# Optimization experiments

Measured on AMD Instinct MI355X. Metric: run time of the kernel, lower is better.

The kernel has to match this reference:

```python
import jax, jax.numpy as jnp
import numpy as np
from jax import lax

VOCAB, D, H, K = 20000, 100, 100, 3
N_U, N_I, R, S, E = 256, 256, 8, 52, 20000


def _text_processor(reviews, emb_table, conv_w, conv_b):
    # reviews: [B,R,S] int -> c: [B,R,S',H]
    B, Rr, Ss = reviews.shape
    embs = emb_table[reviews]                              # [B,R,S,D]
    x = embs.reshape(B * Rr, 1, Ss, D)                     # NCHW
    c = lax.conv_general_dilated(x, conv_w, (1, 1), 'VALID',
                                 dimension_numbers=('NCHW', 'OIHW', 'NCHW'))
    c = jax.nn.relu(c + conv_b[None, :, None, None])       # [B*R,H,S',1]
    Sp = Ss - K + 1
    c = c[..., 0].transpose(0, 2, 1).reshape(B, Rr, Sp, H) # [B,R,S',H]
    return c


def _branch(reviews, emb_table, conv_w, conv_b, fc_w_w, fc_w_b, fc_w2_w, fc_w2_b):
    c = _text_processor(reviews, emb_table, conv_w, conv_b)
    rho = jax.nn.sigmoid(c @ fc_w_w.T + fc_w_b)            # [B,R,S',1]
    z = rho + lax.stop_gradient(jnp.round(rho) - rho)      # straight-through round
    z = z[..., 0]                                          # [B,R,S']
    P = jnp.max(c, axis=-2) @ fc_w2_w.T + fc_w2_b          # [B,R,D]
    return P, z


def reference(user_reviews, item_reviews, uid, iid, emb_table, conv_w, conv_b,
              fc_w_w, fc_w_b, fc_w2_w, fc_w2_b, h_r_w, h_c_w,
              user_bias, item_bias, global_bias):
    P_u, z_u = _branch(user_reviews, emb_table, conv_w, conv_b, fc_w_w, fc_w_b, fc_w2_w, fc_w2_b)
    P_i, z_i = _branch(item_reviews, emb_table, conv_w, conv_b, fc_w_w, fc_w_b, fc_w2_w, fc_w2_b)
    Pu, Pi = P_u[uid], P_i[iid]                            # edge gathers [E,R,D]
    zu, zi = z_u[uid], z_i[iid]                            # [E,R,S']
    s_uv = jnp.einsum('eud,evd->euv', Pu, Pi)              # per-edge review similarity [E,R,R]
    rho_u = jax.nn.sigmoid(s_uv.sum(-1))                   # [E,R]
    rho_v = jax.nn.sigmoid(s_uv.sum(-2))                   # [E,R]
    gamma_u_r = jnp.einsum('ers,er->es', zu, rho_u)        # [E,S']
    gamma_v_r = jnp.einsum('ers,er->es', zi, rho_v)
    pred_r = (jnp.concatenate([gamma_u_r, gamma_v_r], -1) @ h_r_w.T
              + user_bias[uid] + item_bias[iid] + global_bias)  # [E,1]
    gamma_u_c = jnp.einsum('er,erd->ed', rho_u, Pu)        # [E,D]
    gamma_v_c = jnp.einsum('er,erd->ed', rho_v, Pi)
    pred_c = jnp.concatenate([gamma_u_c, gamma_v_c], -1) @ h_c_w.T  # [E,1]
    return pred_r, pred_c, z_u, z_i


def setup_inputs() -> dict:
    key = jax.random.key(0)
    ks = jax.random.split(key, 12)
    return {
        'user_reviews': jax.random.randint(ks[0], (N_U, R, S), 0, VOCAB, dtype=jnp.int32),
        'item_reviews': jax.random.randint(ks[1], (N_I, R, S), 0, VOCAB, dtype=jnp.int32),
        'uid': jax.random.randint(ks[2], (E,), 0, N_U, dtype=jnp.int32),
        'iid': jax.random.randint(ks[3], (E,), 0, N_I, dtype=jnp.int32),
        'emb_table': jax.random.normal(ks[4], (VOCAB, D), jnp.float32) * 0.1,
        'conv_w': jax.random.normal(ks[5], (H, 1, K, D), jnp.float32) * 0.05,
        'conv_b': jnp.zeros((H,), jnp.float32),
        'fc_w_w': jax.random.normal(ks[6], (1, H), jnp.float32) * 0.1,
        'fc_w_b': jnp.zeros((1,), jnp.float32),
        'fc_w2_w': jax.random.normal(ks[7], (D, H), jnp.float32) * 0.1,
        'fc_w2_b': jnp.zeros((D,), jnp.float32),
        'h_r_w': jax.random.normal(ks[8], (1, 2 * (S - K + 1)), jnp.float32) * 0.1,
        'h_c_w': jax.random.normal(ks[9], (1, 2 * D), jnp.float32) * 0.1,
        'user_bias': jnp.zeros((N_U, 1), jnp.float32),
        'item_bias': jnp.zeros((N_I, 1), jnp.float32),
        'global_bias': jnp.zeros((1,), jnp.float32),
    }
```

## Files before the change

kernel.cpp:

```cpp
#include <hip/hip_runtime.h>
#include <hip/hip_fp16.h>
#include <math.h>


typedef __attribute__((ext_vector_type(8))) _Float16 half8;
typedef __attribute__((ext_vector_type(4))) float f32x4;

__device__ __forceinline__ float sigmoidf_(float x) { return 1.f / (1.f + expf(-x)); }
__device__ __forceinline__ ushort f2h(float x) {
    union { __half h; ushort u; } t; t.h = __float2half(x); return t.u;
}
__device__ __forceinline__ float h2f(ushort u) {
    union { __half h; ushort u; } t; t.u = u; return __half2float(t.h);
}

#define Z_MARGIN 4e-4f
#define FLAG_CAP 204800

__global__ void k_prep(const float* __restrict__ conv_w, const float* __restrict__ fc_w2_w,
                       const float* __restrict__ emb,
                       float* __restrict__ Wt, float* __restrict__ fc2t,
                       float* __restrict__ Psum, ushort* __restrict__ wpack,
                       int* __restrict__ flag_cnt, ushort* __restrict__ emb16) {
    int idx = blockIdx.x * 256 + threadIdx.x;
    if (idx < 30000) {
        int kk = idx / 100, h = idx - kk * 100;
        Wt[idx] = conv_w[h * 300 + kk];
    } else if (idx < 40000) {
        int j = idx - 30000;
        int h = j / 100, dd = j - h * 100;
        fc2t[j] = fc_w2_w[dd * 100 + h];
    } else if (idx < 91200) {
        Psum[idx - 40000] = 0.f;
    } else if (idx < 127040) {
        int j = idx - 91200;
        int frag = j >> 9, within = j & 511;
        int l = within >> 3, jj = within & 7;
        int kt = frag / 7, nt = frag % 7;
        int kk = kt * 32 + ((l >> 4) << 3) + jj;
        int h  = nt * 16 + (l & 15);
        wpack[j] = (kk < 300 && h < 100) ? f2h(conv_w[h * 300 + kk]) : (ushort)0;
    } else if (idx == 127040) {
        *flag_cnt = 0;
    } else {
        int j = idx - 127041;
        if (j < 500000) {
            float4 v = ((const float4*)emb)[j];
            uint2 o;
            o.x = (unsigned)f2h(v.x) | ((unsigned)f2h(v.y) << 16);
            o.y = (unsigned)f2h(v.z) | ((unsigned)f2h(v.w) << 16);
            ((uint2*)emb16)[j] = o;
        }
    }
}

__global__ __launch_bounds__(256, 6)
void k_branch(const int* __restrict__ u_rev, const int* __restrict__ i_rev,
              const ushort* __restrict__ emb16, const ushort* __restrict__ wpack,
              const float* __restrict__ conv_b, const float* __restrict__ fc_w_w,
              const float* __restrict__ fc_w_b, const float* __restrict__ fc_w2_b,
              const float* __restrict__ fc2t, const float* __restrict__ h_r_w,
              const float* __restrict__ h_c_w,
              float* __restrict__ Pbuf, float* __restrict__ Psum,
              float* __restrict__ zdot, float* __restrict__ Pdot,
              float* __restrict__ z_out, int* __restrict__ flag_cnt,
              int* __restrict__ flag_list) {
    __shared__ __align__(16) char smem[23552];
    ushort* xw    = (ushort*)smem;
    ushort* wbuf  = (ushort*)(smem + 13312);
    int*    s_tok = (int*)(smem + 20480);
    float*  s_vmax= (float*)(smem + 20688);
    float*  s_maxf= (float*)(smem + 22288);
    float*  s_z   = (float*)(smem + 22688);
    float*  s_lg  = (float*)(smem + 22896);
    float*  s_P   = (float*)(smem + 23104);

    const int tid = threadIdx.x, lane = tid & 63, w = tid >> 6;
    const int gi = blockIdx.x;
    const int branch = gi >> 11, inst = gi & 2047;

    const uint4* wp4 = (const uint4*)wpack;
    uint4* wbuf4 = (uint4*)wbuf;
    uint4 st0 = wp4[tid];
    uint4 st1; if (tid < 192) st1 = wp4[256 + tid];

    const int* rev = branch ? i_rev : u_rev;
    if (tid < 52) s_tok[tid] = rev[inst * 52 + tid];
    __syncthreads();

    {
        const uint2* emb2 = (const uint2*)emb16;
        uint2 v[6];
#pragma unroll
        for (int k = 0; k < 6; k++) {
            int idx = tid + (k << 8);
            if (idx < 1300) {
                int s = idx / 25, c = idx - s * 25;
                v[k] = emb2[s_tok[s] * 25 + c];
            }
        }
#pragma unroll
        for (int k = 0; k < 6; k++) {
            int idx = tid + (k << 8);
            if (idx < 1300) *(uint2*)(xw + idx * 4) = v[k];
        }
        uint4 z4; z4.x = 0u; z4.y = 0u; z4.z = 0u; z4.w = 0u;
        for (int t2 = tid; t2 < 182; t2 += 256)
            ((uint4*)xw)[650 + t2] = z4;
    }

    wbuf4[tid] = st0;
    if (tid < 192) wbuf4[256 + tid] = st1;
    st0 = wp4[448 + tid];
    if (tid < 192) st1 = wp4[448 + 256 + tid];
    __syncthreads();

    f32x4 acc[7];
#pragma unroll
    for (int nt = 0; nt < 7; nt++) acc[nt] = (f32x4){0.f, 0.f, 0.f, 0.f};

    const int col = lane & 15, quad = lane >> 4, q8 = quad << 3;
    const int mt = w;

    for (int kt = 0; kt < 10; kt++) {
        {
            int e0 = (mt * 16 + col) * 100 + kt * 32 + q8;
            union AU { half8 h8; uint2 u2[2]; } a;
            a.u2[0] = *(const uint2*)(xw + e0);
            a.u2[1] = *(const uint2*)(xw + e0 + 4);
#pragma unroll
            for (int nt = 0; nt < 7; nt++) {
                union BU { half8 h8; uint4 u4; } b;
                b.u4 = wbuf4[nt * 64 + lane];
                acc[nt] = __builtin_amdgcn_mfma_f32_16x16x32_f16(a.h8, b.h8, acc[nt], 0, 0, 0);
            }
        }
        __syncthreads();
        if (kt < 9) {
            wbuf4[tid] = st0;
            if (tid < 192) wbuf4[256 + tid] = st1;
            if (kt < 8) {
                st0 = wp4[(kt + 2) * 448 + tid];
                if (tid < 192) st1 = wp4[(kt + 2) * 448 + 256 + tid];
            }
            __syncthreads();
        }
    }

    float cb[7], fw[7], vmax[7];
#pragma unroll
    for (int nt = 0; nt < 7; nt++) {
        int h = nt * 16 + col;
        cb[nt] = (h < 100) ? conv_b[h] : 0.f;
        fw[nt] = (h < 100) ? fc_w_w[h] : 0.f;
        vmax[nt] = 0.f;
    }
    const float fcb = fc_w_b[0];

#pragma unroll
    for (int j = 0; j < 4; j++) {
        int p = mt * 16 + quad * 4 + j;
        bool pv = p < 50;
        float part = 0.f;
#pragma unroll
        for (int nt = 0; nt < 7; nt++) {
            float c = acc[nt][j] + cb[nt];
            c = c > 0.f ? c : 0.f;
            part += c * fw[nt];
            if (pv) vmax[nt] = fmaxf(vmax[nt], c);
        }
        part += __shfl_xor(part, 1, 64);
        part += __shfl_xor(part, 2, 64);
        part += __shfl_xor(part, 4, 64);
        part += __shfl_xor(part, 8, 64);
        if (pv && col == 0) {
            float logit = part + fcb;
            float z = rintf(sigmoidf_(logit));
            s_z[p] = z;
            s_lg[p] = logit;
            z_out[branch * 102400 + inst * 50 + p] = z;
        }
    }

#pragma unroll
    for (int nt = 0; nt < 7; nt++) {
        float m = vmax[nt];
        m = fmaxf(m, __shfl_xor(m, 16, 64));
        m = fmaxf(m, __shfl_xor(m, 32, 64));
        int h = nt * 16 + col;
        if (quad == 0 && h < 100) s_vmax[w * 100 + h] = m;
    }
    __syncthreads();

    if (tid < 100) {
        float mx = fmaxf(fmaxf(s_vmax[tid], s_vmax[100 + tid]),
                         fmaxf(s_vmax[200 + tid], s_vmax[300 + tid]));
        s_maxf[tid] = mx;
    }
    __syncthreads();

    if (tid < 100) {
        float a = fc_w2_b[tid];
        for (int h0 = 0; h0 < 100; h0 += 10) {
            float wv[10], mxv[10];
#pragma unroll
            for (int t = 0; t < 10; t++) {
                wv[t] = fc2t[(h0 + t) * 100 + tid];
                mxv[t] = s_maxf[h0 + t];
            }
#pragma unroll
            for (int t = 0; t < 10; t++) a += mxv[t] * wv[t];
        }
        Pbuf[gi * 100 + tid] = a;
        s_P[tid] = a;
        atomicAdd(&Psum[(branch * 256 + (inst >> 3)) * 100 + tid], a);
    }
    __syncthreads();

    if (w == 0) {
        float v = (lane < 50) ? s_z[lane] * h_r_w[branch * 50 + lane] : 0.f;
        for (int s = 1; s < 64; s <<= 1) v += __shfl_xor(v, s, 64);
        if (lane == 0) zdot[gi] = v;
    } else if (w == 1) {
        float u = 0.f;
        if (lane < 50) u = s_P[lane] * h_c_w[branch * 100 + lane]
                         + s_P[lane + 50] * h_c_w[branch * 100 + lane + 50];
        for (int s = 1; s < 64; s <<= 1) u += __shfl_xor(u, s, 64);
        if (lane == 0) Pdot[gi] = u;
    } else if (w == 2) {
        float lg = 1e9f;
        if (lane < 50) lg = s_lg[lane];
        unsigned long long mb = __ballot(fabsf(lg) < Z_MARGIN);
        int cnt = __popcll(mb);
        int base = 0;
        if (lane == 0 && cnt) base = atomicAdd(flag_cnt, cnt);
        base = __shfl(base, 0, 64);
        if (fabsf(lg) < Z_MARGIN) {
            int rank = __popcll(mb & ((1ull << lane) - 1ull));
            int k = base + rank;
            if (k < FLAG_CAP) flag_list[k] = gi * 50 + lane;
        }
    }
}

__launch_bounds__(256)
__global__ void k_refine(const int* __restrict__ u_rev, const int* __restrict__ i_rev,
                         const float* __restrict__ emb, const float* __restrict__ Wt,
                         const float* __restrict__ conv_b, const float* __restrict__ fc_w_w,
                         const float* __restrict__ fc_w_b, const float* __restrict__ h_r_w,
                         const int* __restrict__ flag_cnt, const int* __restrict__ flag_list,
                         float* __restrict__ z_out, float* __restrict__ zdot) {
    int n = *flag_cnt; if (n > FLAG_CAP) n = FLAG_CAP;
    const int lane = threadIdx.x & 63;
    const int wid = (blockIdx.x * 256 + threadIdx.x) >> 6;
    const int nw = gridDim.x * 4;
    const bool hv = lane < 50;
    const float cb0 = hv ? conv_b[lane] : 0.f;
    const float cb1 = hv ? conv_b[lane + 50] : 0.f;
    const float fw0 = hv ? fc_w_w[lane] : 0.f;
    const float fw1 = hv ? fc_w_w[lane + 50] : 0.f;
    const float fcb = fc_w_b[0];

    for (int e0 = wid * 4; e0 < n; e0 += nw * 4) {
        int gi[4], pos[4];
        bool iv[4];
        float xr[4][5];
#pragma unroll
        for (int m = 0; m < 4; m++) {
            int e = e0 + m;
            iv[m] = e < n;
            int code = iv[m] ? flag_list[e] : 0;
            gi[m] = code / 50; pos[m] = code - gi[m] * 50;
            const int* rev = (gi[m] >> 11) ? i_rev : u_rev;
            int tb = (gi[m] & 2047) * 52 + pos[m];
            int t0 = rev[tb], t1 = rev[tb + 1], t2 = rev[tb + 2];
#pragma unroll
            for (int s = 0; s < 5; s++) {
                int k = s * 64 + lane;
                float v = 0.f;
                if (k < 300) {
                    int r = k / 100, dd = k - r * 100;
                    int t = (r == 0) ? t0 : ((r == 1) ? t1 : t2);
                    v = emb[t * 100 + dd];
                }
                xr[m][s] = v;
            }
        }
        float c0[4], c1[4];
#pragma unroll
        for (int m = 0; m < 4; m++) { c0[m] = cb0; c1[m] = cb1; }
        for (int s = 0; s < 5; s++) {
            const int dmax = (s < 4) ? 64 : 44;
            for (int db = 0; db < dmax; db += 16) {
                const int cnt = (dmax - db < 16) ? (dmax - db) : 16;
                float w0a[16], w1a[16];
#pragma unroll
                for (int t = 0; t < 16; t++) {
                    int d = s * 64 + db + t;
                    bool on = (t < cnt) && hv;
                    w0a[t] = on ? Wt[d * 100 + lane] : 0.f;
                    w1a[t] = on ? Wt[d * 100 + lane + 50] : 0.f;
                }
#pragma unroll
                for (int t = 0; t < 16; t++) {
#pragma unroll
                    for (int m = 0; m < 4; m++) {
                        float x = __shfl(xr[m][s], db + t, 64);
                        c0[m] += x * w0a[t];
                        c1[m] += x * w1a[t];
                    }
                }
            }
        }
#pragma unroll
        for (int m = 0; m < 4; m++) {
            float v = fmaxf(c0[m], 0.f) * fw0 + fmaxf(c1[m], 0.f) * fw1;
            for (int s = 1; s < 64; s <<= 1) v += __shfl_xor(v, s, 64);
            if (lane == 0 && iv[m]) {
                int branch = gi[m] >> 11, inst = gi[m] & 2047;
                float z = rintf(sigmoidf_(v + fcb));
                float old = z_out[branch * 102400 + inst * 50 + pos[m]];
                if (z != old) {
                    z_out[branch * 102400 + inst * 50 + pos[m]] = z;
                    atomicAdd(&zdot[gi[m]], (z - old) * h_r_w[branch * 50 + pos[m]]);
                }
            }
        }
    }
}

__launch_bounds__(256)
__global__ void k_gmat(const float* __restrict__ Pbuf, const float* __restrict__ Psum,
                       ushort* __restrict__ G) {
    __shared__ __align__(16) float sv[100];
    const int b = blockIdx.x, s = b >> 11, i = (b >> 3) & 255, jc = b & 7;
    const int tid = threadIdx.x, lane = tid & 63, w = tid >> 6;
    const float* vec = Psum + (s == 0 ? 25600 : 0) + i * 100;
    if (tid < 100) sv[tid] = vec[tid];
    __syncthreads();
    const int g = lane >> 2, q = lane & 3;
    const float4* rows4 = (const float4*)(Pbuf + s * 204800);
    const float4* sv4 = (const float4*)sv;
    for (int pass = 0; pass < 4; pass++) {
        int j = jc * 256 + pass * 64 + w * 16 + g;
        float part = 0.f;
#pragma unroll
        for (int t = 0; t < 7; t++) {
            int c = q + 4 * t;
            if (c < 25) {
                float4 a = rows4[j * 25 + c], bb = sv4[c];
                part += a.x * bb.x + a.y * bb.y + a.z * bb.z + a.w * bb.w;
            }
        }
        part += __shfl_xor(part, 1, 64);
        part += __shfl_xor(part, 2, 64);
        if (q == 0) G[s * 524288 + i * 2048 + j] = f2h(part);
    }
}

__launch_bounds__(256)
__global__ void k_edge(const int* __restrict__ uid, const int* __restrict__ iid,
                       const ushort* __restrict__ G,
                       const float* __restrict__ zdot, const float* __restrict__ Pdot,
                       const float* __restrict__ user_bias, const float* __restrict__ item_bias,
                       const float* __restrict__ global_bias, float* __restrict__ out) {
    const int tid = threadIdx.x, lane = tid & 63, w = tid >> 6;
    const int e = blockIdx.x * 16 + w * 4 + (lane >> 4);
    const int r = lane & 15;
    int u = uid[e], i = iid[e];
    float gv, wr, wc;
    if (r < 8) {
        gv = h2f(G[i * 2048 + u * 8 + r]);
        wr = zdot[u * 8 + r]; wc = Pdot[u * 8 + r];
    } else {
        int a = r - 8;
        gv = h2f(G[524288 + u * 2048 + i * 8 + a]);
        wr = zdot[2048 + i * 8 + a]; wc = Pdot[2048 + i * 8 + a];
    }
    float sg = sigmoidf_(gv);
    float cr = sg * wr, cc = sg * wc;
    cr += __shfl_xor(cr, 1, 64); cc += __shfl_xor(cc, 1, 64);
    cr += __shfl_xor(cr, 2, 64); cc += __shfl_xor(cc, 2, 64);
    cr += __shfl_xor(cr, 4, 64); cc += __shfl_xor(cc, 4, 64);
    cr += __shfl_xor(cr, 8, 64); cc += __shfl_xor(cc, 8, 64);
    if (r == 0) {
        out[e] = cr + user_bias[u] + item_bias[i] + global_bias[0];
        out[20000 + e] = cc;
    }
}

extern "C" void kernel_launch(void* const* d_in, const int* in_sizes, int n_in,
                              void* d_out, int out_size, void* d_ws, size_t ws_size,
                              hipStream_t stream) {
    const int*   u_rev    = (const int*)d_in[0];
    const int*   i_rev    = (const int*)d_in[1];
    const int*   uid      = (const int*)d_in[2];
    const int*   iid      = (const int*)d_in[3];
    const float* emb      = (const float*)d_in[4];
    const float* conv_w   = (const float*)d_in[5];
    const float* conv_b   = (const float*)d_in[6];
    const float* fc_w_w   = (const float*)d_in[7];
    const float* fc_w_b   = (const float*)d_in[8];
    const float* fc_w2_w  = (const float*)d_in[9];
    const float* fc_w2_b  = (const float*)d_in[10];
    const float* h_r_w    = (const float*)d_in[11];
    const float* h_c_w    = (const float*)d_in[12];
    const float* user_b   = (const float*)d_in[13];
    const float* item_b   = (const float*)d_in[14];
    const float* global_b = (const float*)d_in[15];
    float* out = (float*)d_out;

    float*  ws    = (float*)d_ws;
    float*  Pbuf  = ws;
    float*  Psum  = ws + 409600;
    float*  zdotb = ws + 460800;
    float*  Pdotb = ws + 464896;
    float*  Wt    = ws + 468992;
    float*  fc2t  = ws + 498992;
    ushort* wpack = (ushort*)(ws + 508992);
    int*    flagc = (int*)(ws + 526912);
    int*    flist = (int*)(ws + 526916);
    ushort* emb16 = (ushort*)(ws + 731716);
    ushort* Gbuf  = (ushort*)(ws + 1731716);

    hipLaunchKernelGGL(k_prep, dim3(2450), dim3(256), 0, stream,
                       conv_w, fc_w2_w, emb, Wt, fc2t, Psum, wpack, flagc, emb16);
    hipLaunchKernelGGL(k_branch, dim3(4096), dim3(256), 0, stream,
                       u_rev, i_rev, emb16, wpack, conv_b, fc_w_w, fc_w_b,
                       fc_w2_b, fc2t, h_r_w, h_c_w,
                       Pbuf, Psum, zdotb, Pdotb, out + 40000, flagc, flist);
    hipLaunchKernelGGL(k_refine, dim3(128), dim3(256), 0, stream,
                       u_rev, i_rev, emb, Wt, conv_b, fc_w_w, fc_w_b, h_r_w,
                       flagc, flist, out + 40000, zdotb);
    hipLaunchKernelGGL(k_gmat, dim3(4096), dim3(256), 0, stream, Pbuf, Psum, Gbuf);
    hipLaunchKernelGGL(k_edge, dim3(1250), dim3(256), 0, stream,
                       uid, iid, Gbuf, zdotb, Pdotb,
                       user_b, item_b, global_b, out);
}
```

Measured before the change: 189.2 us.

## Load conv weight fragments directly into registers, dropping LDS staging and barriers

The MFMA B-operand weight fragments are now read straight from global memory (L2/L1-resident) into double-buffered register arrays, prefetching the next k-tile while computing the current one. This removes the LDS weight buffer and the two block-wide barriers per k-step, which shrinks shared memory from 23.5KB to 16KB. Launch bounds drop from 6 to 4 waves per SIMD to leave room for the 14 extra uint4 registers, trading occupancy for fewer syncs. Each wave now fetches the full weight set redundantly from cache.

Measured after the change: 205.3 us. 1.09x slower.

```diff
diff --git a/kernel.cpp b/kernel.cpp
--- a/kernel.cpp
+++ b/kernel.cpp
@@ -54,7 +54,7 @@
     }
 }
 
-__global__ __launch_bounds__(256, 6)
+__global__ __launch_bounds__(256, 4)
 void k_branch(const int* __restrict__ u_rev, const int* __restrict__ i_rev,
               const ushort* __restrict__ emb16, const ushort* __restrict__ wpack,
               const float* __restrict__ conv_b, const float* __restrict__ fc_w_w,
@@ -65,24 +65,20 @@
               float* __restrict__ zdot, float* __restrict__ Pdot,
               float* __restrict__ z_out, int* __restrict__ flag_cnt,
               int* __restrict__ flag_list) {
-    __shared__ __align__(16) char smem[23552];
+    __shared__ __align__(16) char smem[16384];
     ushort* xw    = (ushort*)smem;
-    ushort* wbuf  = (ushort*)(smem + 13312);
-    int*    s_tok = (int*)(smem + 20480);
-    float*  s_vmax= (float*)(smem + 20688);
-    float*  s_maxf= (float*)(smem + 22288);
-    float*  s_z   = (float*)(smem + 22688);
-    float*  s_lg  = (float*)(smem + 22896);
-    float*  s_P   = (float*)(smem + 23104);
+    int*    s_tok = (int*)(smem + 13312);
+    float*  s_vmax= (float*)(smem + 13520);
+    float*  s_maxf= (float*)(smem + 15120);
+    float*  s_z   = (float*)(smem + 15520);
+    float*  s_lg  = (float*)(smem + 15728);
+    float*  s_P   = (float*)(smem + 15936);
 
     const int tid = threadIdx.x, lane = tid & 63, w = tid >> 6;
     const int gi = blockIdx.x;
     const int branch = gi >> 11, inst = gi & 2047;
 
     const uint4* wp4 = (const uint4*)wpack;
-    uint4* wbuf4 = (uint4*)wbuf;
-    uint4 st0 = wp4[tid];
-    uint4 st1; if (tid < 192) st1 = wp4[256 + tid];
 
     const int* rev = branch ? i_rev : u_rev;
     if (tid < 52) s_tok[tid] = rev[inst * 52 + tid];
@@ -108,11 +104,6 @@
         for (int t2 = tid; t2 < 182; t2 += 256)
             ((uint4*)xw)[650 + t2] = z4;
     }
-
-    wbuf4[tid] = st0;
-    if (tid < 192) wbuf4[256 + tid] = st1;
-    st0 = wp4[448 + tid];
-    if (tid < 192) st1 = wp4[448 + 256 + tid];
     __syncthreads();
 
     f32x4 acc[7];
@@ -122,30 +113,41 @@
     const int col = lane & 15, quad = lane >> 4, q8 = quad << 3;
     const int mt = w;
 
-    for (int kt = 0; kt < 10; kt++) {
-        {
-            int e0 = (mt * 16 + col) * 100 + kt * 32 + q8;
-            union AU { half8 h8; uint2 u2[2]; } a;
-            a.u2[0] = *(const uint2*)(xw + e0);
-            a.u2[1] = *(const uint2*)(xw + e0 + 4);
-#pragma unroll
-            for (int nt = 0; nt < 7; nt++) {
-                union BU { half8 h8; uint4 u4; } b;
-                b.u4 = wbuf4[nt * 64 + lane];
-                acc[nt] = __builtin_amdgcn_mfma_f32_16x16x32_f16(a.h8, b.h8, acc[nt], 0, 0, 0);
-            }
-        }
-        __syncthreads();
-        if (kt < 9) {
-            wbuf4[tid] = st0;
-            if (tid < 192) wbuf4[256 + tid] = st1;
-            if (kt < 8) {
-                st0 = wp4[(kt + 2) * 448 + tid];
-                if (tid < 192) st1 = wp4[(kt + 2) * 448 + 256 + tid];
-            }
-            __syncthreads();
-        }
-    }
+    uint4 bA[7], bB[7];
+#pragma unroll
+    for (int nt = 0; nt < 7; nt++) bA[nt] = wp4[nt * 64 + lane];
+
+#define KT_BODY(KT, CUR, NXT)                                                   \
+    {                                                                           \
+        if ((KT) < 9) {                                                         \
+            _Pragma("unroll")                                                   \
+            for (int nt = 0; nt < 7; nt++)                                      \
+                NXT[nt] = wp4[((KT) + 1) * 448 + nt * 64 + lane];               \
+        }                                                                       \
+        int e0 = (mt * 16 + col) * 100 + (KT) * 32 + q8;                        \
+        union AU { half8 h8; uint2 u2[2]; } a;                                  \
+        a.u2[0] = *(const uint2*)(xw + e0);                                     \
+        a.u2[1] = *(const uint2*)(xw + e0 + 4);                                 \
+        _Pragma("unroll")                                                       \
+        for (int nt = 0; nt < 7; nt++) {                                        \
+            union BV { half8 h8; uint4 u4; } b;                                 \
+            b.u4 = CUR[nt];                                                     \
+            acc[nt] = __builtin_amdgcn_mfma_f32_16x16x32_f16(a.h8, b.h8,        \
+                                                             acc[nt], 0, 0, 0); \
+        }                                                                       \
+    }
+
+    KT_BODY(0, bA, bB)
+    KT_BODY(1, bB, bA)
+    KT_BODY(2, bA, bB)
+    KT_BODY(3, bB, bA)
+    KT_BODY(4, bA, bB)
+    KT_BODY(5, bB, bA)
+    KT_BODY(6, bA, bB)
+    KT_BODY(7, bB, bA)
+    KT_BODY(8, bA, bB)
+    KT_BODY(9, bB, bA)
+#undef KT_BODY
 
     float cb[7], fw[7], vmax[7];
 #pragma unroll
```

## Process two review instances per k_branch block to reuse staged conv weights

Applied to the files above, without the earlier changes.

Each k_branch block now handles two review instances instead of one, so the grid is halved. The fp16 conv weight tiles staged into LDS are loaded once and feed MFMAs for both instances, which halves global weight traffic and barrier count per instance. In exchange the block needs roughly twice the LDS and twice the accumulator registers, and launch bounds drop to 4 waves-per-EU, so occupancy falls.

Measured after the change: 184.9 us. 1.02x faster.

```diff
diff --git a/kernel.cpp b/kernel.cpp
--- a/kernel.cpp
+++ b/kernel.cpp
@@ -54,7 +54,7 @@
     }
 }
 
-__global__ __launch_bounds__(256, 6)
+__global__ __launch_bounds__(256, 4)
 void k_branch(const int* __restrict__ u_rev, const int* __restrict__ i_rev,
               const ushort* __restrict__ emb16, const ushort* __restrict__ wpack,
               const float* __restrict__ conv_b, const float* __restrict__ fc_w_w,
@@ -65,19 +65,20 @@
               float* __restrict__ zdot, float* __restrict__ Pdot,
               float* __restrict__ z_out, int* __restrict__ flag_cnt,
               int* __restrict__ flag_list) {
-    __shared__ __align__(16) char smem[23552];
+    __shared__ __align__(16) char smem[39840];
     ushort* xw    = (ushort*)smem;
-    ushort* wbuf  = (ushort*)(smem + 13312);
-    int*    s_tok = (int*)(smem + 20480);
-    float*  s_vmax= (float*)(smem + 20688);
-    float*  s_maxf= (float*)(smem + 22288);
-    float*  s_z   = (float*)(smem + 22688);
-    float*  s_lg  = (float*)(smem + 22896);
-    float*  s_P   = (float*)(smem + 23104);
+    ushort* wbuf  = (ushort*)(smem + 26624);
+    int*    s_tok = (int*)(smem + 33792);
+    float*  s_vmax= (float*)(smem + 34208);
+    float*  s_maxf= (float*)(smem + 37408);
+    float*  s_z   = (float*)(smem + 38208);
+    float*  s_lg  = (float*)(smem + 38624);
+    float*  s_P   = (float*)(smem + 39040);
 
     const int tid = threadIdx.x, lane = tid & 63, w = tid >> 6;
-    const int gi = blockIdx.x;
-    const int branch = gi >> 11, inst = gi & 2047;
+    const int b = blockIdx.x;
+    const int branch = b >> 10, pair = b & 1023;
+    const int inst0 = pair * 2;
 
     const uint4* wp4 = (const uint4*)wpack;
     uint4* wbuf4 = (uint4*)wbuf;
@@ -85,28 +86,39 @@
     uint4 st1; if (tid < 192) st1 = wp4[256 + tid];
 
     const int* rev = branch ? i_rev : u_rev;
-    if (tid < 52) s_tok[tid] = rev[inst * 52 + tid];
+    if (tid < 104) {
+        int ii = tid >= 52, s = tid - ii * 52;
+        s_tok[tid] = rev[(inst0 + ii) * 52 + s];
+    }
     __syncthreads();
 
     {
         const uint2* emb2 = (const uint2*)emb16;
-        uint2 v[6];
-#pragma unroll
-        for (int k = 0; k < 6; k++) {
+        uint2 v[11];
+#pragma unroll
+        for (int k = 0; k < 11; k++) {
             int idx = tid + (k << 8);
-            if (idx < 1300) {
-                int s = idx / 25, c = idx - s * 25;
-                v[k] = emb2[s_tok[s] * 25 + c];
-            }
-        }
-#pragma unroll
-        for (int k = 0; k < 6; k++) {
+            if (idx < 2600) {
+                int ii = idx >= 1300;
+                int within = idx - ii * 1300;
+                int s = within / 25, c = within - s * 25;
+                v[k] = emb2[s_tok[ii * 52 + s] * 25 + c];
+            }
+        }
+#pragma unroll
+        for (int k = 0; k < 11; k++) {
             int idx = tid + (k << 8);
-            if (idx < 1300) *(uint2*)(xw + idx * 4) = v[k];
+            if (idx < 2600) {
+                int ii = idx >= 1300;
+                int within = idx - ii * 1300;
+                *(uint2*)(xw + ii * 6656 + within * 4) = v[k];
+            }
         }
         uint4 z4; z4.x = 0u; z4.y = 0u; z4.z = 0u; z4.w = 0u;
-        for (int t2 = tid; t2 < 182; t2 += 256)
-            ((uint4*)xw)[650 + t2] = z4;
+        for (int t2 = tid; t2 < 364; t2 += 256) {
+            int ii = t2 >= 182, off = t2 - ii * 182;
+            ((uint4*)xw)[ii * 832 + 650 + off] = z4;
+        }
     }
 
     wbuf4[tid] = st0;
@@ -115,9 +127,12 @@
     if (tid < 192) st1 = wp4[448 + 256 + tid];
     __syncthreads();
 
-    f32x4 acc[7];
-#pragma unroll
-    for (int nt = 0; nt < 7; nt++) acc[nt] = (f32x4){0.f, 0.f, 0.f, 0.f};
+    f32x4 acc0[7], acc1[7];
+#pragma unroll
+    for (int nt = 0; nt < 7; nt++) {
+        acc0[nt] = (f32x4){0.f, 0.f, 0.f, 0.f};
+        acc1[nt] = (f32x4){0.f, 0.f, 0.f, 0.f};
+    }
 
     const int col = lane & 15, quad = lane >> 4, q8 = quad << 3;
     const int mt = w;
@@ -125,14 +140,17 @@
     for (int kt = 0; kt < 10; kt++) {
         {
             int e0 = (mt * 16 + col) * 100 + kt * 32 + q8;
-            union AU { half8 h8; uint2 u2[2]; } a;
-            a.u2[0] = *(const uint2*)(xw + e0);
-            a.u2[1] = *(const uint2*)(xw + e0 + 4);
+            union AU { half8 h8; uint2 u2[2]; } a0, a1;
+            a0.u2[0] = *(const uint2*)(xw + e0);
+            a0.u2[1] = *(const uint2*)(xw + e0 + 4);
+            a1.u2[0] = *(const uint2*)(xw + 6656 + e0);
+            a1.u2[1] = *(const uint2*)(xw + 6656 + e0 + 4);
 #pragma unroll
             for (int nt = 0; nt < 7; nt++) {
-                union BU { half8 h8; uint4 u4; } b;
-                b.u4 = wbuf4[nt * 64 + lane];
-                acc[nt] = __builtin_amdgcn_mfma_f32_16x16x32_f16(a.h8, b.h8, acc[nt], 0, 0, 0);
+                union BU { half8 h8; uint4 u4; } bu;
+                bu.u4 = wbuf4[nt * 64 + lane];
+                acc0[nt] = __builtin_amdgcn_mfma_f32_16x16x32_f16(a0.h8, bu.h8, acc0[nt], 0, 0, 0);
+                acc1[nt] = __builtin_amdgcn_mfma_f32_16x16x32_f16(a1.h8, bu.h8, acc1[nt], 0, 0, 0);
             }
         }
         __syncthreads();
@@ -147,89 +165,108 @@
         }
     }
 
-    float cb[7], fw[7], vmax[7];
+    float cb[7], fw[7];
 #pragma unroll
     for (int nt = 0; nt < 7; nt++) {
         int h = nt * 16 + col;
         cb[nt] = (h < 100) ? conv_b[h] : 0.f;
         fw[nt] = (h < 100) ? fc_w_w[h] : 0.f;
-        vmax[nt] = 0.f;
     }
     const float fcb = fc_w_b[0];
 
-#pragma unroll
-    for (int j = 0; j < 4; j++) {
-        int p = mt * 16 + quad * 4 + j;
-        bool pv = p < 50;
-        float part = 0.f;
-#pragma unroll
-        for (int nt = 0; nt < 7; nt++) {
-            float c = acc[nt][j] + cb[nt];
-            c = c > 0.f ? c : 0.f;
-            part += c * fw[nt];
-            if (pv) vmax[nt] = fmaxf(vmax[nt], c);
-        }
-        part += __shfl_xor(part, 1, 64);
-        part += __shfl_xor(part, 2, 64);
-        part += __shfl_xor(part, 4, 64);
-        part += __shfl_xor(part, 8, 64);
-        if (pv && col == 0) {
-            float logit = part + fcb;
-            float z = rintf(sigmoidf_(logit));
-            s_z[p] = z;
-            s_lg[p] = logit;
-            z_out[branch * 102400 + inst * 50 + p] = z;
-        }
-    }
-
-#pragma unroll
-    for (int nt = 0; nt < 7; nt++) {
-        float m = vmax[nt];
-        m = fmaxf(m, __shfl_xor(m, 16, 64));
-        m = fmaxf(m, __shfl_xor(m, 32, 64));
-        int h = nt * 16 + col;
-        if (quad == 0 && h < 100) s_vmax[w * 100 + h] = m;
-    }
-    __syncthreads();
-
-    if (tid < 100) {
-        float mx = fmaxf(fmaxf(s_vmax[tid], s_vmax[100 + tid]),
-                         fmaxf(s_vmax[200 + tid], s_vmax[300 + tid]));
-        s_maxf[tid] = mx;
-    }
-    __syncthreads();
-
-    if (tid < 100) {
-        float a = fc_w2_b[tid];
+#define EPILOGUE_MM(II, ACC)                                                   \
+    {                                                                          \
+        float vmax[7];                                                         \
+        _Pragma("unroll") for (int nt = 0; nt < 7; nt++) vmax[nt] = 0.f;       \
+        _Pragma("unroll")                                                      \
+        for (int j = 0; j < 4; j++) {                                          \
+            int p = mt * 16 + quad * 4 + j;                                    \
+            bool pv = p < 50;                                                  \
+            float part = 0.f;                                                  \
+            _Pragma("unroll")                                                  \
+            for (int nt = 0; nt < 7; nt++) {                                   \
+                float c = ACC[nt][j] + cb[nt];                                 \
+                c = c > 0.f ? c : 0.f;                                         \
+                part += c * fw[nt];                                            \
+                if (pv) vmax[nt] = fmaxf(vmax[nt], c);                         \
+            }                                                                  \
+            part += __shfl_xor(part, 1, 64);                                   \
+            part += __shfl_xor(part, 2, 64);                                   \
+            part += __shfl_xor(part, 4, 64);                                   \
+            part += __shfl_xor(part, 8, 64);                                   \
+            if (pv && col == 0) {                                              \
+                float logit = part + fcb;                                      \
+                float z = rintf(sigmoidf_(logit));                             \
+                s_z[(II) * 52 + p] = z;                                        \
+                s_lg[(II) * 52 + p] = logit;                                   \
+                z_out[branch * 102400 + (inst0 + (II)) * 50 + p] = z;          \
+            }                                                                  \
+        }                                                                      \
+        _Pragma("unroll")                                                      \
+        for (int nt = 0; nt < 7; nt++) {                                       \
+            float m = vmax[nt];                                                \
+            m = fmaxf(m, __shfl_xor(m, 16, 64));                               \
+            m = fmaxf(m, __shfl_xor(m, 32, 64));                               \
+            int h = nt * 16 + col;                                             \
+            if (quad == 0 && h < 100) s_vmax[(II) * 400 + w * 100 + h] = m;    \
+        }                                                                      \
+    }
+
+    EPILOGUE_MM(0, acc0)
+    EPILOGUE_MM(1, acc1)
+#undef EPILOGUE_MM
+    __syncthreads();
+
+    if (tid < 200) {
+        int ii = tid >= 100, h = tid - ii * 100;
+        const float* sv = s_vmax + ii * 400;
+        float mx = fmaxf(fmaxf(sv[h], sv[100 + h]),
+                         fmaxf(sv[200 + h], sv[300 + h]));
+        s_maxf[ii * 100 + h] = mx;
+    }
+    __syncthreads();
+
+    if (tid < 200) {
+        int ii = tid >= 100, dd = tid - ii * 100;
+        float a = fc_w2_b[dd];
         for (int h0 = 0; h0 < 100; h0 += 10) {
             float wv[10], mxv[10];
 #pragma unroll
             for (int t = 0; t < 10; t++) {
-                wv[t] = fc2t[(h0 + t) * 100 + tid];
-                mxv[t] = s_maxf[h0 + t];
+                wv[t] = fc2t[(h0 + t) * 100 + dd];
+                mxv[t] = s_maxf[ii * 100 + h0 + t];
             }
 #pragma unroll
             for (int t = 0; t < 10; t++) a += mxv[t] * wv[t];
         }
-        Pbuf[gi * 100 + tid] = a;
-        s_P[tid] = a;
-        atomicAdd(&Psum[(branch * 256 + (inst >> 3)) * 100 + tid], a);
+        int inst = inst0 + ii;
+        int gi = branch * 2048 + inst;
+        Pbuf[gi * 100 + dd] = a;
+        s_P[ii * 100 + dd] = a;
+        atomicAdd(&Psum[(branch * 256 + (inst >> 3)) * 100 + dd], a);
     }
     __syncthreads();
 
     if (w == 0) {
-        float v = (lane < 50) ? s_z[lane] * h_r_w[branch * 50 + lane] : 0.f;
-        for (int s = 1; s < 64; s <<= 1) v += __shfl_xor(v, s, 64);
-        if (lane == 0) zdot[gi] = v;
+#pragma unroll
+        for (int ii = 0; ii < 2; ii++) {
+            float v = (lane < 50) ? s_z[ii * 52 + lane] * h_r_w[branch * 50 + lane] : 0.f;
+            for (int s = 1; s < 64; s <<= 1) v += __shfl_xor(v, s, 64);
+            if (lane == 0) zdot[branch * 2048 + inst0 + ii] = v;
+        }
     } else if (w == 1) {
-        float u = 0.f;
-        if (lane < 50) u = s_P[lane] * h_c_w[branch * 100 + lane]
-                         + s_P[lane + 50] * h_c_w[branch * 100 + lane + 50];
-        for (int s = 1; s < 64; s <<= 1) u += __shfl_xor(u, s, 64);
-        if (lane == 0) Pdot[gi] = u;
-    } else if (w == 2) {
+#pragma unroll
+        for (int ii = 0; ii < 2; ii++) {
+            float u = 0.f;
+            if (lane < 50) u = s_P[ii * 100 + lane] * h_c_w[branch * 100 + lane]
+                             + s_P[ii * 100 + lane + 50] * h_c_w[branch * 100 + lane + 50];
+            for (int s = 1; s < 64; s <<= 1) u += __shfl_xor(u, s, 64);
+            if (lane == 0) Pdot[branch * 2048 + inst0 + ii] = u;
+        }
+    } else {
+        int ii = w - 2;
         float lg = 1e9f;
-        if (lane < 50) lg = s_lg[lane];
+        if (lane < 50) lg = s_lg[ii * 52 + lane];
         unsigned long long mb = __ballot(fabsf(lg) < Z_MARGIN);
         int cnt = __popcll(mb);
         int base = 0;
@@ -238,7 +275,7 @@
         if (fabsf(lg) < Z_MARGIN) {
             int rank = __popcll(mb & ((1ull << lane) - 1ull));
             int k = base + rank;
-            if (k < FLAG_CAP) flag_list[k] = gi * 50 + lane;
+            if (k < FLAG_CAP) flag_list[k] = (branch * 2048 + inst0 + ii) * 50 + lane;
         }
     }
 }
@@ -425,7 +462,7 @@
 
     hipLaunchKernelGGL(k_prep, dim3(2450), dim3(256), 0, stream,
                        conv_w, fc_w2_w, emb, Wt, fc2t, Psum, wpack, flagc, emb16);
-    hipLaunchKernelGGL(k_branch, dim3(4096), dim3(256), 0, stream,
+    hipLaunchKernelGGL(k_branch, dim3(2048), dim3(256), 0, stream,
                        u_rev, i_rev, emb16, wpack, conv_b, fc_w_w, fc_w_b,
                        fc_w2_b, fc2t, h_r_w, h_c_w,
                        Pbuf, Psum, zdotb, Pdotb, out + 40000, flagc, flist);
```
